# Performance work log

Hardware: AMD Instinct MI355X
Metric: run time of the kernel (lower is better)

Reference implementation:

```python
import jax, jax.numpy as jnp
import numpy as np

TOP_K = 2
N_EXPERTS = 8


def setup_inputs() -> dict:
    key = jax.random.key(0)
    k1, k2, k3 = jax.random.split(key, 3)
    B, S, D, O, E = 2, 4096, 1024, 1024, N_EXPERTS
    scale_in = 1.0 / np.sqrt(D)
    return {
        "x": jax.random.normal(k1, (B, S, D), dtype=jnp.float32),
        "gate_w": jax.random.normal(k2, (E, D), dtype=jnp.float32) * scale_in,
        "gate_b": jnp.zeros((E,), dtype=jnp.float32),
        "expert_w": jax.random.normal(k3, (E, O, D), dtype=jnp.float32) * scale_in,
        "expert_b": jnp.zeros((E, O), dtype=jnp.float32),
    }


def reference(x, gate_w, gate_b, expert_w, expert_b):
    B, S, D = x.shape
    E, O, _ = expert_w.shape
    h = x.reshape(-1, D)  # [T, D] flattened tokens

    # Router: logits -> float32 softmax -> top-k -> renormalized weights
    router_logits = h @ gate_w.T + gate_b  # [T, E]
    probs = jax.nn.softmax(router_logits.astype(jnp.float32), axis=-1)
    topk_w, topk_idx = jax.lax.top_k(probs, TOP_K)  # [T, K]
    topk_w = topk_w / jnp.sum(topk_w, axis=-1, keepdims=True)
    topk_w = topk_w.astype(h.dtype)

    # Dense combine weights per (token, expert): zero for unselected experts.
    combine = jnp.sum(
        jax.nn.one_hot(topk_idx, E, dtype=h.dtype) * topk_w[..., None], axis=1
    )  # [T, E]

    # All-expert outputs, then weighted combine (math-equivalent to
    # per-expert gather-GEMM-scatter since combine is 0 off the top-k).
    expert_out = jnp.einsum("td,eod->teo", h, expert_w) + expert_b[None]  # [T, E, O]
    out = jnp.einsum("te,teo->to", combine, expert_out)  # [T, O]

    return out.reshape(B, S, O), router_logits
```

## Files before the change

### kernel.cpp

```cpp
#include <hip/hip_runtime.h>
#include <hip/hip_bf16.h>
#include <stdint.h>

typedef __attribute__((ext_vector_type(8))) short bf16x8;
typedef __attribute__((ext_vector_type(4))) float f32x4;

#define T_TOKENS 8192
#define DIM 1024
#define NEXP 8
#define NPAIR 28
#define BUFSZ 40960

__device__ __forceinline__ unsigned short f2bf(float f) {
  unsigned u = __float_as_uint(f);
  u = (u + 0x7FFFu + ((u >> 16) & 1u)) >> 16;
  return (unsigned short)u;
}

__global__ __launch_bounds__(256) void router_kernel(
    const float* __restrict__ x, const float* __restrict__ gw, const float* __restrict__ gb,
    float* __restrict__ logits_out, unsigned short* __restrict__ xw,
    int* __restrict__ tk_e, float* __restrict__ tk_w) {
  int wave = threadIdx.x >> 6, lane = threadIdx.x & 63;
  int t = blockIdx.x * 4 + wave;
  float acc[NEXP];
#pragma unroll
  for (int e = 0; e < NEXP; ++e) acc[e] = 0.f;
  const float4* xr = (const float4*)(x + (size_t)t * DIM);
  ushort4* xo = (ushort4*)(xw + (size_t)t * DIM);
#pragma unroll
  for (int it = 0; it < 4; ++it) {
    int d4 = it * 64 + lane;
    float4 xv = xr[d4];
    ushort4 xb;
    xb.x = f2bf(xv.x); xb.y = f2bf(xv.y); xb.z = f2bf(xv.z); xb.w = f2bf(xv.w);
    xo[d4] = xb;
#pragma unroll
    for (int e = 0; e < NEXP; ++e) {
      float4 gv = ((const float4*)(gw + e * DIM))[d4];
      acc[e] += xv.x * gv.x + xv.y * gv.y + xv.z * gv.z + xv.w * gv.w;
    }
  }
#pragma unroll
  for (int off = 32; off; off >>= 1)
#pragma unroll
    for (int e = 0; e < NEXP; ++e) acc[e] += __shfl_xor(acc[e], off);
  if (lane == 0) {
    float4 gb0 = ((const float4*)gb)[0];
    float4 gb1 = ((const float4*)gb)[1];
    acc[0] += gb0.x; acc[1] += gb0.y; acc[2] += gb0.z; acc[3] += gb0.w;
    acc[4] += gb1.x; acc[5] += gb1.y; acc[6] += gb1.z; acc[7] += gb1.w;
    float4* lp = (float4*)(logits_out + (size_t)t * NEXP);
    lp[0] = make_float4(acc[0], acc[1], acc[2], acc[3]);
    lp[1] = make_float4(acc[4], acc[5], acc[6], acc[7]);
    int e0 = 0; float l0 = acc[0];
#pragma unroll
    for (int e = 1; e < NEXP; ++e) if (acc[e] > l0) { l0 = acc[e]; e0 = e; }
    int e1 = -1; float l1 = -1e30f;
#pragma unroll
    for (int e = 0; e < NEXP; ++e) if (e != e0 && acc[e] > l1) { l1 = acc[e]; e1 = e; }
    float r = expf(l1 - l0);
    float w0 = 1.f / (1.f + r);
    float w1 = r * w0;
    tk_e[t * 2] = e0; tk_e[t * 2 + 1] = e1;
    tk_w[t * 2] = w0; tk_w[t * 2 + 1] = w1;
  }
}

__global__ __launch_bounds__(1024) void sortconv_kernel(
    const float* __restrict__ ew, unsigned short* __restrict__ w_bf,
    const int* __restrict__ tk_e, const float* __restrict__ tk_w,
    int* __restrict__ offsets_g, int* __restrict__ row_tok,
    float2* __restrict__ row_wab, int* __restrict__ pairAB_g,
    int* __restrict__ tiles_g, int* __restrict__ n_tiles_g) {
  if (blockIdx.x > 0) {
    int i = (blockIdx.x - 1) * 1024 + threadIdx.x;
    float4 v = ((const float4*)ew)[i];
    ushort4 o;
    o.x = f2bf(v.x); o.y = f2bf(v.y); o.z = f2bf(v.z); o.w = f2bf(v.w);
    ((ushort4*)w_bf)[i] = o;
    return;
  }
  int tid = threadIdx.x;
  int lane = tid & 63, wv = tid >> 6;
  __shared__ unsigned short excl16[NPAIR][1024];
  __shared__ int wavebase[16][NPAIR];
  __shared__ int offs_l[NPAIR + 1];

  int pp[8];
  float wa_[8], wb_[8];
  const int base = tid * 8;
#pragma unroll
  for (int i = 0; i < 8; ++i) {
    int2 ev = ((const int2*)tk_e)[base + i];
    float2 wv2 = ((const float2*)tk_w)[base + i];
    int a, b;
    float wa, wb;
    if (ev.x < ev.y) { a = ev.x; b = ev.y; wa = wv2.x; wb = wv2.y; }
    else             { a = ev.y; b = ev.x; wa = wv2.y; wb = wv2.x; }
    pp[i] = a * (15 - a) / 2 + (b - a - 1);
    wa_[i] = wa; wb_[i] = wb;
  }

#pragma unroll
  for (int p = 0; p < NPAIR; ++p) {
    int cnt = 0;
#pragma unroll
    for (int i = 0; i < 8; ++i) cnt += (pp[i] == p);
    int incl = cnt;
#pragma unroll
    for (int off = 1; off < 64; off <<= 1) {
      int n = __shfl_up(incl, off);
      if (lane >= off) incl += n;
    }
    excl16[p][tid] = (unsigned short)(incl - cnt);
    if (lane == 63) wavebase[wv][p] = incl;
  }
  __syncthreads();

  if (wv == 0 && lane < NPAIR) {
    const int p = lane;
    int tot = 0;
#pragma unroll
    for (int w = 0; w < 16; ++w) {
      int v = wavebase[w][p];
      wavebase[w][p] = tot;
      tot += v;
    }
    int incl = tot;
#pragma unroll
    for (int off = 1; off < 32; off <<= 1) {
      int n = __shfl_up(incl, off);
      if (lane >= off) incl += n;
    }
    int exc = incl - tot;
    offs_l[p] = exc;
    offsets_g[p] = exc;
    if (p == NPAIR - 1) { offs_l[NPAIR] = incl; offsets_g[NPAIR] = incl; }
    int a = 0, b = 0, bse = 0;
#pragma unroll
    for (int aa = 0; aa < 7; ++aa) {
      int sz = 7 - aa;
      if (p >= bse && p < bse + sz) { a = aa; b = aa + 1 + (p - bse); }
      bse += sz;
    }
    pairAB_g[p] = a | (b << 4);
    int mt = (tot + 127) >> 7;
    int tcnt = 2 * mt;
    int tincl = tcnt;
#pragma unroll
    for (int off = 1; off < 32; off <<= 1) {
      int n = __shfl_up(tincl, off);
      if (lane >= off) tincl += n;
    }
    int tbase = tincl - tcnt;
    for (int n = 0; n < 2; ++n)
      for (int m = 0; m < mt; ++m) tiles_g[tbase + n * mt + m] = p | (n << 5) | (m << 6);
    if (p == NPAIR - 1) {
      n_tiles_g[0] = tincl;
      n_tiles_g[1] = (tincl + 7) >> 3;
    }
  }
  __syncthreads();

#pragma unroll
  for (int i = 0; i < 8; ++i) {
    int p = pp[i];
    int rank = 0;
#pragma unroll
    for (int j = 0; j < 8; ++j)
      if (j < i) rank += (pp[j] == p);
    int pos = offs_l[p] + wavebase[wv][p] + (int)excl16[p][tid] + rank;
    row_tok[pos] = base + i;
    row_wab[pos] = make_float2(wa_[i], wb_[i]);
  }
}

#define GLOAD16(g, l)                                                                   \
  __builtin_amdgcn_global_load_lds((const __attribute__((address_space(1))) unsigned int*)(g), \
                                   (__attribute__((address_space(3))) unsigned int*)(l), 16, 0, 0)

__global__ __launch_bounds__(512, 2) void gemm_kernel(
    const unsigned short* __restrict__ xw, const unsigned short* __restrict__ w_bf,
    const int* __restrict__ row_tok, const float2* __restrict__ row_wab,
    const int* __restrict__ offsets, const int* __restrict__ pairAB,
    const int* __restrict__ tiles, const int* __restrict__ n_tiles,
    const float* __restrict__ eb, float* __restrict__ out) {
  const int nb = n_tiles[0], cpx = n_tiles[1];
  const int wg = blockIdx.x;
  const int slot = wg >> 3;
  if (slot >= cpx) return;
  const int idx = (wg & 7) * cpx + slot;
  if (idx >= nb) return;
  const int s = tiles[idx];
  const int pid = s & 31;
  const int n0 = ((s >> 5) & 1) << 9;
  const int m0 = (s >> 6) << 7;
  const int ab = pairAB[pid];
  const int ea = ab & 15, ebx = ab >> 4;
  const int seg0 = offsets[pid], segN = offsets[pid + 1] - seg0;

  const int tid = threadIdx.x;
  const int lane = tid & 63, wave = tid >> 6;
  const int wr = wave >> 2, wc = wave & 3;

  __shared__ __align__(16) char smem[3 * BUFSZ];

  const int arow = tid >> 2;
  const int swzc = ((tid & 3) ^ ((tid >> 3) & 3)) << 4;
  const int dA = tid * 16;
  const int dB = 8192 + tid * 16;

  int gr0 = m0 + arow; if (gr0 > segN - 1) gr0 = segN - 1;
  const char* srcA = (const char*)xw + (size_t)row_tok[seg0 + gr0] * 2048 + swzc;
  const char* srcBa = (const char*)w_bf + (((size_t)ea << 20) + (size_t)(n0 + arow) * 1024) * 2 + swzc;
  const char* srcBb = (const char*)w_bf + (((size_t)ebx << 20) + (size_t)(n0 + arow) * 1024) * 2 + swzc;

  float rat[4][4], wav[4][4], wbe[4][4];
#pragma unroll
  for (int m = 0; m < 4; ++m) {
#pragma unroll
    for (int r = 0; r < 4; ++r) {
      int g = m0 + wr * 64 + m * 16 + ((lane >> 4) << 2) + r;
      if (g > segN - 1) g = segN - 1;
      float2 wab = row_wab[seg0 + g];
      float we = fmaxf(wab.y, 1e-20f);
      wav[m][r] = wab.x;
      wbe[m][r] = we;
      rat[m][r] = wab.x / we;
    }
  }

  const int rsw = (((lane >> 4) ^ (lane >> 1)) & 3) << 4;
  int aoff[4], boff[8];
#pragma unroll
  for (int m = 0; m < 4; ++m)
    aoff[m] = (wr * 64 + m * 16 + (lane & 15)) * 64 + rsw;
#pragma unroll
  for (int n = 0; n < 8; ++n)
    boff[n] = 8192 + (wc * 128 + n * 16 + (lane & 15)) * 64 + rsw;

  f32x4 acc[4][8];
#pragma unroll
  for (int m = 0; m < 4; ++m)
#pragma unroll
    for (int n = 0; n < 8; ++n) acc[m][n] = (f32x4){0.f, 0.f, 0.f, 0.f};

#define STAGE5(bufo, pa, pb)                                   \
  {                                                            \
    GLOAD16((pa), smem + (bufo) + dA);                         \
    GLOAD16((pb), smem + (bufo) + dB);                         \
    GLOAD16((pb) + 262144, smem + (bufo) + dB + 8192);         \
    GLOAD16((pb) + 524288, smem + (bufo) + dB + 16384);        \
    GLOAD16((pb) + 786432, smem + (bufo) + dB + 24576);        \
  }
#define STAGEJ(bufo, j)                                                  \
  {                                                                      \
    if ((j) < 32) { const int kb = (j) * 64;                             \
      STAGE5(bufo, srcA + kb, srcBa + kb); }                             \
    else { const int kb = ((j) - 32) * 64;                               \
      STAGE5(bufo, srcA + kb, srcBb + kb); }                             \
  }

  STAGEJ(0, 0);
  STAGEJ(BUFSZ, 1);

  int cb = 0;
  for (int kt = 0; kt < 64; ++kt) {
    if (kt < 63) {
      asm volatile("s_waitcnt vmcnt(5)" ::: "memory");
    } else {
      asm volatile("s_waitcnt vmcnt(0)" ::: "memory");
    }
    __builtin_amdgcn_s_barrier();
    const int cur = cb * BUFSZ;
    bf16x8 a_[4], b_[8];
#pragma unroll
    for (int m = 0; m < 4; ++m) a_[m] = *(const bf16x8*)(smem + cur + aoff[m]);
#pragma unroll
    for (int n = 0; n < 8; ++n) b_[n] = *(const bf16x8*)(smem + cur + boff[n]);
    if (kt < 62) {
      int cbn = cb + 2; if (cbn >= 3) cbn -= 3;
      STAGEJ(cbn * BUFSZ, kt + 2);
    }
    if (kt == 32) {
#pragma unroll
      for (int m = 0; m < 4; ++m)
#pragma unroll
        for (int n = 0; n < 8; ++n)
#pragma unroll
          for (int r = 0; r < 4; ++r) acc[m][n][r] *= rat[m][r];
    }
    __builtin_amdgcn_s_setprio(1);
#pragma unroll
    for (int m = 0; m < 4; ++m)
#pragma unroll
      for (int n = 0; n < 8; ++n)
        acc[m][n] = __builtin_amdgcn_mfma_f32_16x16x32_bf16(a_[m], b_[n], acc[m][n], 0, 0, 0);
    __builtin_amdgcn_s_setprio(0);
    cb = (cb + 1 == 3) ? 0 : cb + 1;
  }

  const float* ba = eb + ea * 1024;
  const float* bb = eb + ebx * 1024;
#pragma unroll
  for (int m = 0; m < 4; ++m) {
#pragma unroll
    for (int r = 0; r < 4; ++r) {
      int g = m0 + wr * 64 + m * 16 + ((lane >> 4) << 2) + r;
      if (g < segN) {
        int p = seg0 + g;
        float wa = wav[m][r], we = wbe[m][r];
        int token = row_tok[p];
        float* op = out + (size_t)token * 1024;
#pragma unroll
        for (int n = 0; n < 8; ++n) {
          int col = n0 + wc * 128 + n * 16 + (lane & 15);
          op[col] = we * acc[m][n][r] + wa * ba[col] + we * bb[col];
        }
      }
    }
  }
#undef STAGEJ
#undef STAGE5
}

extern "C" void kernel_launch(void* const* d_in, const int* in_sizes, int n_in,
                              void* d_out, int out_size, void* d_ws, size_t ws_size,
                              hipStream_t stream) {
  const float* x  = (const float*)d_in[0];
  const float* gw = (const float*)d_in[1];
  const float* gb = (const float*)d_in[2];
  const float* ew = (const float*)d_in[3];
  const float* eb = (const float*)d_in[4];
  float* out = (float*)d_out;
  float* logits = out + (size_t)T_TOKENS * 1024;

  char* ws = (char*)d_ws;
  unsigned short* xw   = (unsigned short*)(ws);
  unsigned short* w_bf = (unsigned short*)(ws + 16777216);
  int*    tk_e     = (int*)(ws + 33554432);
  float*  tk_w     = (float*)(ws + 33619968);
  int*    row_tok  = (int*)(ws + 33685504);
  float2* row_wab  = (float2*)(ws + 33751040);
  int*    offsets  = (int*)(ws + 33816576);
  int*    pairAB   = (int*)(ws + 33816704);
  int*    n_tiles  = (int*)(ws + 33816832);
  int*    tiles    = (int*)(ws + 33816960);

  router_kernel<<<2048, 256, 0, stream>>>(x, gw, gb, logits, xw, tk_e, tk_w);
  sortconv_kernel<<<2049, 1024, 0, stream>>>(ew, w_bf, tk_e, tk_w, offsets, row_tok,
                                             row_wab, pairAB, tiles, n_tiles);
  gemm_kernel<<<256, 512, 0, stream>>>(xw, w_bf, row_tok, row_wab, offsets, pairAB,
                                       tiles, n_tiles, eb, out);
}
```

Before: 99.65 us.

## Process two K-steps per barrier with four-buffer LDS ping-pong pipeline

Replaces the three-buffer, one-K-tile-per-iteration pipeline with a four-buffer scheme. Each iteration consumes two K tiles and prefetches the next two into the other buffer pair. This halves the number of barriers and waitcnt points per tile. In exchange it waits for all outstanding loads (vmcnt 0) each iteration, which reduces the overlap depth, and it raises LDS usage to 160KB per workgroup, which may reduce occupancy.

```diff
diff --git a/kernel.cpp b/kernel.cpp
--- a/kernel.cpp
+++ b/kernel.cpp
@@ -204,7 +204,7 @@
   const int lane = tid & 63, wave = tid >> 6;
   const int wr = wave >> 2, wc = wave & 3;
 
-  __shared__ __align__(16) char smem[3 * BUFSZ];
+  __shared__ __align__(16) char smem[4 * BUFSZ];
 
   const int arow = tid >> 2;
   const int swzc = ((tid & 3) ^ ((tid >> 3) & 3)) << 4;
@@ -265,40 +265,54 @@
   STAGEJ(0, 0);
   STAGEJ(BUFSZ, 1);
 
-  int cb = 0;
-  for (int kt = 0; kt < 64; ++kt) {
-    if (kt < 63) {
-      asm volatile("s_waitcnt vmcnt(5)" ::: "memory");
-    } else {
-      asm volatile("s_waitcnt vmcnt(0)" ::: "memory");
-    }
+  for (int w = 0; w < 32; ++w) {
+    asm volatile("s_waitcnt vmcnt(0)" ::: "memory");
     __builtin_amdgcn_s_barrier();
-    const int cur = cb * BUFSZ;
-    bf16x8 a_[4], b_[8];
-#pragma unroll
-    for (int m = 0; m < 4; ++m) a_[m] = *(const bf16x8*)(smem + cur + aoff[m]);
-#pragma unroll
-    for (int n = 0; n < 8; ++n) b_[n] = *(const bf16x8*)(smem + cur + boff[n]);
-    if (kt < 62) {
-      int cbn = cb + 2; if (cbn >= 3) cbn -= 3;
-      STAGEJ(cbn * BUFSZ, kt + 2);
-    }
-    if (kt == 32) {
+    const int pb = (w & 1) << 1;
+    const int cur0 = pb * BUFSZ;
+    const int cur1 = (pb + 1) * BUFSZ;
+    const int ob = pb ^ 2;
+
+    {
+      bf16x8 a_[4], b_[8];
+#pragma unroll
+      for (int m = 0; m < 4; ++m) a_[m] = *(const bf16x8*)(smem + cur0 + aoff[m]);
+#pragma unroll
+      for (int n = 0; n < 8; ++n) b_[n] = *(const bf16x8*)(smem + cur0 + boff[n]);
+      if (w < 31) {
+        STAGEJ(ob * BUFSZ, 2 * w + 2);
+        STAGEJ((ob + 1) * BUFSZ, 2 * w + 3);
+      }
+      if (w == 16) {
+#pragma unroll
+        for (int m = 0; m < 4; ++m)
+#pragma unroll
+          for (int n = 0; n < 8; ++n)
+#pragma unroll
+            for (int r = 0; r < 4; ++r) acc[m][n][r] *= rat[m][r];
+      }
+      __builtin_amdgcn_s_setprio(1);
 #pragma unroll
       for (int m = 0; m < 4; ++m)
 #pragma unroll
         for (int n = 0; n < 8; ++n)
-#pragma unroll
-          for (int r = 0; r < 4; ++r) acc[m][n][r] *= rat[m][r];
-    }
-    __builtin_amdgcn_s_setprio(1);
-#pragma unroll
-    for (int m = 0; m < 4; ++m)
-#pragma unroll
-      for (int n = 0; n < 8; ++n)
-        acc[m][n] = __builtin_amdgcn_mfma_f32_16x16x32_bf16(a_[m], b_[n], acc[m][n], 0, 0, 0);
-    __builtin_amdgcn_s_setprio(0);
-    cb = (cb + 1 == 3) ? 0 : cb + 1;
+          acc[m][n] = __builtin_amdgcn_mfma_f32_16x16x32_bf16(a_[m], b_[n], acc[m][n], 0, 0, 0);
+      __builtin_amdgcn_s_setprio(0);
+    }
+    {
+      bf16x8 a_[4], b_[8];
+#pragma unroll
+      for (int m = 0; m < 4; ++m) a_[m] = *(const bf16x8*)(smem + cur1 + aoff[m]);
+#pragma unroll
+      for (int n = 0; n < 8; ++n) b_[n] = *(const bf16x8*)(smem + cur1 + boff[n]);
+      __builtin_amdgcn_s_setprio(1);
+#pragma unroll
+      for (int m = 0; m < 4; ++m)
+#pragma unroll
+        for (int n = 0; n < 8; ++n)
+          acc[m][n] = __builtin_amdgcn_mfma_f32_16x16x32_bf16(a_[m], b_[n], acc[m][n], 0, 0, 0);
+      __builtin_amdgcn_s_setprio(0);
+    }
   }
 
   const float* ba = eb + ea * 1024;
```

Measured after the change: 109.5 us. +9.9%, slower.
